# Kernel tuning notes

Measured on AMD Instinct MI355X. Metric: run time of the kernel, lower is better.

## Reference

```python
import jax, jax.numpy as jnp
import numpy as np
from jax import lax

B, H, W = 2, 384, 384
NF = 64
SECTIONS = [2, 3, 4, 5, 6, 7, 8]  # radial core widths -> kernel sizes 3,5,7,9,11,13,15


def _radial_matrix(w):
    """Static [K,K,w] matrix mapping w radial core channels -> full KxK kernel,
    K = 2*w-1, replicating the torch nested-loop radial interpolation + flipcat."""
    mid = w - 1
    M = np.zeros((w, w, w), dtype=np.float32)
    for i in range(w):
        for j in range(w):
            d = np.sqrt(float((i - mid) ** 2 + (j - mid) ** 2))
            if d > mid:
                continue
            low, high = np.floor(d), np.ceil(d)
            if low == high:
                M[i, j, int(low)] = 1.0
            else:
                M[i, j, int(low)] = high - d
                M[i, j, int(low) + 1] = d - low
    # flipcat along both spatial dims: index order [0..w-1, w-2..0]
    q = mid - np.abs(np.arange(2 * w - 1) - mid)
    return M[q][:, q]  # [K, K, w]


def _conv(x, w, b):
    y = lax.conv_general_dilated(x, w, (1, 1), 'SAME',
                                 dimension_numbers=('NCHW', 'OIHW', 'NCHW'))
    return y + b[None, :, None, None]


def _resblock(x, wa, ba, wb, bb):
    return x + _conv(jax.nn.relu(_conv(x, wa, ba)), wb, bb)


def setup_inputs() -> dict:
    key = jax.random.key(0)
    ks = jax.random.split(key, 12)

    def wgt(k, shape):
        fan_in = shape[1] * shape[2] * shape[3]
        return jax.random.normal(k, shape, jnp.float32) / np.sqrt(fan_in)

    inp = {
        'data_with_est': jax.random.normal(ks[0], (B, 2, H, W), jnp.float32),
        'data': jax.random.normal(ks[1], (B, 1, H, W), jnp.float32),
        'w_first': wgt(ks[2], (NF, 2, 3, 3)), 'b_first': jnp.zeros((NF,), jnp.float32),
        'w1a': wgt(ks[3], (NF, NF, 3, 3)), 'b1a': jnp.zeros((NF,), jnp.float32),
        'w1b': wgt(ks[4], (NF, NF, 3, 3)), 'b1b': jnp.zeros((NF,), jnp.float32),
        'w2a': wgt(ks[5], (NF, NF, 3, 3)), 'b2a': jnp.zeros((NF,), jnp.float32),
        'w2b': wgt(ks[6], (NF, NF, 3, 3)), 'b2b': jnp.zeros((NF,), jnp.float32),
        'w3a': wgt(ks[7], (NF, NF, 3, 3)), 'b3a': jnp.zeros((NF,), jnp.float32),
        'w3b': wgt(ks[8], (NF, NF, 3, 3)), 'b3b': jnp.zeros((NF,), jnp.float32),
        'w_out': wgt(ks[9], (35, NF, 3, 3)), 'b_out': jnp.zeros((35,), jnp.float32),
    }
    return inp


def reference(data_with_est, data, w_first, b_first, w1a, b1a, w1b, b1b,
              w2a, b2a, w2b, b2b, w3a, b3a, w3b, b3b, w_out, b_out):
    # KPN backbone
    x = _conv(data_with_est, w_first, b_first)
    x = _resblock(x, w1a, b1a, w1b, b1b)
    x = _resblock(x, w2a, b2a, w2b, b2b)
    x = _resblock(x, w3a, b3a, w3b, b3b)
    core = _conv(x, w_out, b_out)  # [B, 35, H, W]

    frames = data[:, 0]  # [B, H, W]  (N=1, color=1)
    pred_img = jnp.zeros((B, H, W), core.dtype)
    off = 0
    for wsec in SECTIONS:
        K = 2 * wsec - 1
        r = K // 2
        M = jnp.asarray(_radial_matrix(wsec))  # [K, K, wsec]
        c = jnp.abs(lax.slice_in_dim(core, off, off + wsec, axis=1))  # [B, wsec, H, W]
        off += wsec
        # position-varying KxK kernel per pixel, softmax over the K*K taps
        kern = jnp.einsum('ijc,bchw->bijhw', M, c).reshape(B, K * K, H, W)
        kern = jax.nn.softmax(kern, axis=1)
        pad = jnp.pad(frames, ((0, 0), (r, r), (r, r)))
        # shifted neighborhood stack in torch loop order (i over rows, j over cols)
        patches = jnp.stack([pad[:, i:i + H, j:j + W]
                             for i in range(K) for j in range(K)], axis=1)
        pred_img = pred_img + jnp.sum(kern * patches, axis=1)
    return pred_img[:, None]  # [B, 1, H, W]
```

## Files before the change

kernel.cpp:

```cpp
#include <hip/hip_runtime.h>

#define HH 384
#define WW 384
#define BB 2

typedef unsigned short ushort_t;
typedef short  s16x8 __attribute__((ext_vector_type(8)));
typedef float  f32x4 __attribute__((ext_vector_type(4)));
typedef int    i32x4 __attribute__((ext_vector_type(4)));
typedef int    i32x2 __attribute__((ext_vector_type(2)));

union V16 { i32x4 i4; s16x8 v; ushort_t h[8]; };
union V8  { i32x2 i2; ushort_t h[4]; };

__device__ __forceinline__ ushort_t f2b(float f) {
    unsigned u = __builtin_bit_cast(unsigned, f);
    u += 0x7fffu + ((u >> 16) & 1u);
    return (ushort_t)(u >> 16);
}
__device__ __forceinline__ float b2f(ushort_t h) {
    return __builtin_bit_cast(float, ((unsigned)h) << 16);
}

struct WSrc { const float* p[8]; };

__global__ __launch_bounds__(256)
void repack_k(WSrc ws, ushort_t* __restrict__ Wd)
{
    const int idx = blockIdx.x * 256 + threadIdx.x;
    float val = 0.f;
    if (idx < 221184) {
        const int j = idx / 36864, rem = idx - j * 36864;
        const int i = rem & 7, lane = (rem >> 3) & 63;
        const int f = rem >> 9;
        const int mt = f & 3, st = f >> 2;
        const int t = st % 9, s = st / 9;
        const int co = mt * 16 + (lane & 15);
        const int ci = s * 32 + (lane >> 4) * 8 + i;
        val = ws.p[j][((size_t)(co * 64 + ci)) * 9 + t];
    } else if (idx < 248832) {
        const int rem = idx - 221184;
        const int i = rem & 7, lane = (rem >> 3) & 63;
        const int f = rem >> 9;
        const int mt = f % 3, st = f / 3;
        const int t = st % 9, s = st / 9;
        const int co = mt * 16 + (lane & 15);
        const int ci = s * 32 + (lane >> 4) * 8 + i;
        val = (co < 35) ? ws.p[6][((size_t)(co * 64 + ci)) * 9 + t] : 0.f;
    } else {
        const int rem = idx - 248832;
        const int i = rem & 7, lane = (rem >> 3) & 63;
        const int mt = rem >> 9;
        const int co = mt * 16 + (lane & 15);
        const int k = (lane >> 4) * 8 + i;
        if (k < 18) {
            const int ch = (k >= 9) ? 1 : 0;
            const int t = k - ch * 9;
            val = ws.p[7][((size_t)(co * 2 + ch)) * 9 + t];
        }
    }
    if (idx < 250880) Wd[idx] = f2b(val);
}

template<bool RELU, bool RES>
__global__ __launch_bounds__(256, 2)
void conv_mfma(const ushort_t* __restrict__ in, const ushort_t* __restrict__ wp,
               const float* __restrict__ bias, const ushort_t* __restrict__ res,
               ushort_t* __restrict__ out)
{
    __shared__ __align__(16) char smem[41472 + 36864];
    i32x4* s4 = (i32x4*)smem;
    i32x4* sw = (i32x4*)(smem + 41472);

    const int tid = threadIdx.x;
    const int x0 = blockIdx.x * 16, y0 = blockIdx.y * 16, b = blockIdx.z;
    const int lane = tid & 63, w4 = (tid >> 6) * 4;
    const int n = lane & 15, g = lane >> 4;

    {
        i32x4 ta[11];
#pragma unroll
        for (int k = 0; k < 11; ++k) {
            const int idx = tid + k * 256;
            ta[k] = 0;
            if (idx < 2592) {
                const int oct = idx & 7, p = idx >> 3;
                const int r = p / 18, xx = p - r * 18;
                const int gy = y0 - 1 + r, gx = x0 - 1 + xx;
                if ((unsigned)gy < HH && (unsigned)gx < WW)
                    ta[k] = *(const i32x4*)(in +
                        ((size_t)((b * HH + gy) * WW + gx)) * 64 + oct * 8);
            }
        }
        i32x4 tw[9];
#pragma unroll
        for (int k = 0; k < 9; ++k)
            tw[k] = *(const i32x4*)(wp + (size_t)(tid + k * 256) * 8);
#pragma unroll
        for (int k = 0; k < 11; ++k) {
            const int idx = tid + k * 256;
            if (idx < 2592) {
                const int oct = idx & 7, p = idx >> 3;
                const int r = p / 18, xx = p - r * 18;
                s4[(r * 8 + oct) * 18 + xx] = ta[k];
            }
        }
#pragma unroll
        for (int k = 0; k < 9; ++k)
            sw[tid + k * 256] = tw[k];
    }
    __syncthreads();

    f32x4 acc[4][4];
#pragma unroll
    for (int i = 0; i < 4; ++i)
#pragma unroll
        for (int j = 0; j < 4; ++j) acc[i][j] = 0.f;

    i32x4 pw[9];
#pragma unroll
    for (int k = 0; k < 9; ++k)
        pw[k] = *(const i32x4*)(wp + (size_t)(2304 + tid + k * 256) * 8);

#pragma unroll
    for (int t = 0; t < 9; ++t) {
        const int ky = t / 3, kx = t - ky * 3;
        V16 bf[4];
#pragma unroll
        for (int nt = 0; nt < 4; ++nt)
            bf[nt].i4 = s4[((w4 + nt + ky) * 8 + g) * 18 + (n + kx)];
#pragma unroll
        for (int mt = 0; mt < 4; ++mt) {
            V16 af; af.i4 = sw[(t * 4 + mt) * 64 + lane];
#pragma unroll
            for (int nt = 0; nt < 4; ++nt)
                acc[nt][mt] = __builtin_amdgcn_mfma_f32_16x16x32_bf16(
                    af.v, bf[nt].v, acc[nt][mt], 0, 0, 0);
        }
    }

    __syncthreads();
#pragma unroll
    for (int k = 0; k < 9; ++k)
        sw[tid + k * 256] = pw[k];
    __syncthreads();

#pragma unroll
    for (int t = 0; t < 9; ++t) {
        const int ky = t / 3, kx = t - ky * 3;
        V16 bf[4];
#pragma unroll
        for (int nt = 0; nt < 4; ++nt)
            bf[nt].i4 = s4[((w4 + nt + ky) * 8 + 4 + g) * 18 + (n + kx)];
#pragma unroll
        for (int mt = 0; mt < 4; ++mt) {
            V16 af; af.i4 = sw[(t * 4 + mt) * 64 + lane];
#pragma unroll
            for (int nt = 0; nt < 4; ++nt)
                acc[nt][mt] = __builtin_amdgcn_mfma_f32_16x16x32_bf16(
                    af.v, bf[nt].v, acc[nt][mt], 0, 0, 0);
        }
    }

    __syncthreads();
#pragma unroll
    for (int nt = 0; nt < 4; ++nt) {
        const int row = w4 + nt;
#pragma unroll
        for (int mt = 0; mt < 4; ++mt) {
            const int co0 = mt * 16 + g * 4;
            const float4 bv = *(const float4*)(bias + co0);
            float vv[4] = {acc[nt][mt][0] + bv.x, acc[nt][mt][1] + bv.y,
                           acc[nt][mt][2] + bv.z, acc[nt][mt][3] + bv.w};
            V8 ov;
#pragma unroll
            for (int r = 0; r < 4; ++r)
                ov.h[r] = f2b(RELU ? fmaxf(vv[r], 0.f) : vv[r]);
            const int c = 2 * mt + (g >> 1);
            const int cpr = c ^ (n & 7);
            *(i32x2*)(smem + row * 2048 + n * 128 + cpr * 16 + (g & 1) * 8) = ov.i2;
        }
    }
    __syncthreads();
#pragma unroll
    for (int r0 = 0; r0 < 4; ++r0) {
        const int row = w4 + r0, y = y0 + row;
#pragma unroll
        for (int j = 0; j < 2; ++j) {
            const int px = (lane >> 3) + 8 * j;
            const int clin = lane & 7;
            const int cpr = clin ^ (px & 7);
            V16 v;
            v.i4 = *(const i32x4*)(smem + row * 2048 + px * 128 + cpr * 16);
            const size_t goff = ((size_t)((b * HH + y) * WW + x0 + px)) * 64
                                + clin * 8;
            if (RES) {
                V16 rv;
                rv.i4 = *(const i32x4*)(res + goff);
#pragma unroll
                for (int e = 0; e < 8; ++e)
                    v.h[e] = f2b(b2f(v.h[e]) + b2f(rv.h[e]));
            }
            *(i32x4*)(out + goff) = v.i4;
        }
    }
}

__global__ __launch_bounds__(256, 4)
void conv_first(const float* __restrict__ in, const ushort_t* __restrict__ wp,
                const float* __restrict__ bias, ushort_t* __restrict__ out)
{
    __shared__ float s_raw[2][18][20];
    __shared__ __align__(16) char epi[32768];
    const int tid = threadIdx.x;
    const int x0 = blockIdx.x * 16, y0 = blockIdx.y * 16, b = blockIdx.z;
    {
        float tmp[3];
#pragma unroll
        for (int k = 0; k < 3; ++k) {
            const int idx = tid + k * 256;
            tmp[k] = 0.f;
            if (idx < 648) {
                const int ch = idx / 324, rem = idx - ch * 324;
                const int r = rem / 18, x = rem - r * 18;
                const int gy = y0 - 1 + r, gx = x0 - 1 + x;
                if ((unsigned)gy < HH && (unsigned)gx < WW)
                    tmp[k] = in[((size_t)((b * 2 + ch) * HH + gy)) * WW + gx];
            }
        }
#pragma unroll
        for (int k = 0; k < 3; ++k) {
            const int idx = tid + k * 256;
            if (idx < 648) {
                const int ch = idx / 324, rem = idx - ch * 324;
                const int r = rem / 18, x = rem - r * 18;
                s_raw[ch][r][x] = tmp[k];
            }
        }
    }
    __syncthreads();

    const int lane = tid & 63, w4 = (tid >> 6) * 4;
    const int n = lane & 15, g = lane >> 4;

    V16 af[4];
#pragma unroll
    for (int mt = 0; mt < 4; ++mt)
        af[mt].i4 = *(const i32x4*)(wp + ((size_t)(mt * 64 + lane)) * 8);

    f32x4 acc[4][4];
#pragma unroll
    for (int i = 0; i < 4; ++i)
#pragma unroll
        for (int j = 0; j < 4; ++j) acc[i][j] = 0.f;

#pragma unroll
    for (int nt = 0; nt < 4; ++nt) {
        const int r = w4 + nt;
        V16 bf;
#pragma unroll
        for (int i = 0; i < 8; ++i) {
            const int k = g * 8 + i;
            float v = 0.f;
            if (k < 18) {
                const int ch = (k >= 9) ? 1 : 0;
                const int t = k - ch * 9;
                const int ky = t / 3, kx = t - ky * 3;
                v = s_raw[ch][r + ky][n + kx];
            }
            bf.h[i] = f2b(v);
        }
#pragma unroll
        for (int mt = 0; mt < 4; ++mt)
            acc[nt][mt] = __builtin_amdgcn_mfma_f32_16x16x32_bf16(
                af[mt].v, bf.v, acc[nt][mt], 0, 0, 0);
    }

#pragma unroll
    for (int nt = 0; nt < 4; ++nt) {
        const int row = w4 + nt;
#pragma unroll
        for (int mt = 0; mt < 4; ++mt) {
            const int co0 = mt * 16 + g * 4;
            const float4 bv = *(const float4*)(bias + co0);
            V8 ov;
            ov.h[0] = f2b(acc[nt][mt][0] + bv.x);
            ov.h[1] = f2b(acc[nt][mt][1] + bv.y);
            ov.h[2] = f2b(acc[nt][mt][2] + bv.z);
            ov.h[3] = f2b(acc[nt][mt][3] + bv.w);
            const int c = 2 * mt + (g >> 1);
            const int cpr = c ^ (n & 7);
            *(i32x2*)(epi + row * 2048 + n * 128 + cpr * 16 + (g & 1) * 8) = ov.i2;
        }
    }
    __syncthreads();
#pragma unroll
    for (int r0 = 0; r0 < 4; ++r0) {
        const int row = w4 + r0, y = y0 + row;
#pragma unroll
        for (int j = 0; j < 2; ++j) {
            const int px = (lane >> 3) + 8 * j;
            const int clin = lane & 7;
            const int cpr = clin ^ (px & 7);
            i32x4 v = *(const i32x4*)(epi + row * 2048 + px * 128 + cpr * 16);
            *(i32x4*)(out + ((size_t)((b * HH + y) * WW + x0 + px)) * 64
                          + clin * 8) = v;
        }
    }
}

constexpr int isq_(int v) { int r = 0; while ((r + 1) * (r + 1) <= v) ++r; return r; }
constexpr double csqrt_(int x) {
    double g = x ? (double)x : 0.0;
    if (x) for (int i = 0; i < 80; ++i) g = 0.5 * (g + (double)x / g);
    return g;
}
constexpr int tapm_(int W, int d2) {
    const int R = W - 1; int c = 0;
    for (int di = -R; di <= R; ++di)
        for (int dj = -R; dj <= R; ++dj)
            if (di * di + dj * dj == d2) ++c;
    return c;
}
constexpr int nout_(int W) {
    const int R = W - 1; int c = 0;
    for (int di = -R; di <= R; ++di)
        for (int dj = -R; dj <= R; ++dj)
            if (di * di + dj * dj > R * R) ++c;
    return c;
}

template<int W, int D2, int DI>
struct DiSum {
    static constexpr int R = W - 1;
    static __device__ __forceinline__ float run(const float* s_f, int base) {
        float s = 0.f;
        constexpr int rem = D2 - DI * DI;
        if constexpr (rem >= 0) {
            constexpr int sj = isq_(rem >= 0 ? rem : 0);
            if constexpr (sj * sj == rem) {
                s += s_f[base + DI * 48 + sj];
                if constexpr (sj > 0) s += s_f[base + DI * 48 - sj];
            }
        }
        if constexpr (DI < R) s += DiSum<W, D2, DI + 1>::run(s_f, base);
        return s;
    }
};

template<int W, int OFF, int D2>
struct D2Loop {
    static __device__ __forceinline__ void run(const float* cv, const float* s_f,
                                               int base, float& num, float& den) {
        constexpr int m = tapm_(W, D2);
        if constexpr (m > 0) {
            constexpr int lo = isq_(D2);
            float v;
            if constexpr (lo * lo == D2) {
                v = cv[OFF + lo];
            } else {
                constexpr float fr = (float)(csqrt_(D2) - (double)lo);
                v = __builtin_fmaf(fr, cv[OFF + lo + 1] - cv[OFF + lo], cv[OFF + lo]);
            }
            const float e = __expf(v);
            const float S = DiSum<W, D2, -(W - 1)>::run(s_f, base);
            num = __builtin_fmaf(e, S, num);
            den = __builtin_fmaf((float)m, e, den);
        }
        if constexpr (D2 > 0)
            D2Loop<W, OFF, D2 - 1>::run(cv, s_f, base, num, den);
    }
};

template<int W, int OFF>
__device__ __forceinline__ float kpn_section(const float* cv, const float* s_f,
                                             int base)
{
    constexpr int R = W - 1, R2 = R * R;
    float sout = 0.f;
#pragma unroll
    for (int di = -R; di <= R; ++di)
#pragma unroll
        for (int dj = -R; dj <= R; ++dj)
            if (di * di + dj * dj > R2)
                sout += s_f[base + di * 48 + dj];
    float num = sout, den = (float)nout_(W);
    D2Loop<W, OFF, R2>::run(cv, s_f, base, num, den);
    return num / den;
}

__global__ __launch_bounds__(256, 2)
void conv_kpn(const ushort_t* __restrict__ in, const ushort_t* __restrict__ wp,
              const float* __restrict__ bias, const float* __restrict__ frames,
              float* __restrict__ out)
{
    __shared__ __align__(16) char smem[41472 + 5760 + 27648];
    i32x4* s4 = (i32x4*)smem;
    float* s_core = (float*)smem;
    float* s_f = (float*)(smem + 41472);
    i32x4* sw = (i32x4*)(smem + 41472 + 5760);

    const int tid = threadIdx.x;
    const int x0 = blockIdx.x * 16, y0 = blockIdx.y * 16, b = blockIdx.z;

    {
        i32x4 ta[11];
#pragma unroll
        for (int k = 0; k < 11; ++k) {
            const int idx = tid + k * 256;
            ta[k] = 0;
            if (idx < 2592) {
                const int oct = idx & 7, p = idx >> 3;
                const int r = p / 18, xx = p - r * 18;
                const int gy = y0 - 1 + r, gx = x0 - 1 + xx;
                if ((unsigned)gy < HH && (unsigned)gx < WW)
                    ta[k] = *(const i32x4*)(in +
                        ((size_t)((b * HH + gy) * WW + gx)) * 64 + oct * 8);
            }
        }
        float ff[4];
#pragma unroll
        for (int k = 0; k < 4; ++k) {
            const int idx = tid + k * 256;
            ff[k] = 0.f;
            if (idx < 900) {
                const int r = idx / 30, c = idx - r * 30;
                const int y = y0 - 7 + r, x = x0 - 7 + c;
                if ((unsigned)y < HH && (unsigned)x < WW)
                    ff[k] = frames[((size_t)b * HH + y) * WW + x];
            }
        }
        i32x4 tw[7];
#pragma unroll
        for (int k = 0; k < 7; ++k) {
            const int idx = tid + k * 256;
            tw[k] = 0;
            if (idx < 1728)
                tw[k] = *(const i32x4*)(wp + (size_t)idx * 8);
        }
#pragma unroll
        for (int k = 0; k < 11; ++k) {
            const int idx = tid + k * 256;
            if (idx < 2592) {
                const int oct = idx & 7, p = idx >> 3;
                const int r = p / 18, xx = p - r * 18;
                s4[(r * 8 + oct) * 18 + xx] = ta[k];
            }
        }
#pragma unroll
        for (int k = 0; k < 4; ++k) {
            const int idx = tid + k * 256;
            if (idx < 900) {
                const int r = idx / 30, c = idx - r * 30;
                s_f[r * 48 + c] = ff[k];
            }
        }
#pragma unroll
        for (int k = 0; k < 7; ++k) {
            const int idx = tid + k * 256;
            if (idx < 1728) sw[idx] = tw[k];
        }
    }
    __syncthreads();

    const int lane = tid & 63, w4 = (tid >> 6) * 4;
    const int n = lane & 15, g = lane >> 4;

    f32x4 acc[4][3];
#pragma unroll
    for (int i = 0; i < 4; ++i)
#pragma unroll
        for (int j = 0; j < 3; ++j) acc[i][j] = 0.f;

    i32x4 pw[7];
#pragma unroll
    for (int k = 0; k < 7; ++k) {
        const int idx = tid + k * 256;
        pw[k] = 0;
        if (idx < 1728)
            pw[k] = *(const i32x4*)(wp + (size_t)(1728 + idx) * 8);
    }

#pragma unroll
    for (int t = 0; t < 9; ++t) {
        const int ky = t / 3, kx = t - ky * 3;
        V16 bf[4];
#pragma unroll
        for (int nt = 0; nt < 4; ++nt)
            bf[nt].i4 = s4[((w4 + nt + ky) * 8 + g) * 18 + (n + kx)];
#pragma unroll
        for (int mt = 0; mt < 3; ++mt) {
            V16 af; af.i4 = sw[(t * 3 + mt) * 64 + lane];
#pragma unroll
            for (int nt = 0; nt < 4; ++nt)
                acc[nt][mt] = __builtin_amdgcn_mfma_f32_16x16x32_bf16(
                    af.v, bf[nt].v, acc[nt][mt], 0, 0, 0);
        }
    }

    __syncthreads();
#pragma unroll
    for (int k = 0; k < 7; ++k) {
        const int idx = tid + k * 256;
        if (idx < 1728) sw[idx] = pw[k];
    }
    __syncthreads();

#pragma unroll
    for (int t = 0; t < 9; ++t) {
        const int ky = t / 3, kx = t - ky * 3;
        V16 bf[4];
#pragma unroll
        for (int nt = 0; nt < 4; ++nt)
            bf[nt].i4 = s4[((w4 + nt + ky) * 8 + 4 + g) * 18 + (n + kx)];
#pragma unroll
        for (int mt = 0; mt < 3; ++mt) {
            V16 af; af.i4 = sw[(t * 3 + mt) * 64 + lane];
#pragma unroll
            for (int nt = 0; nt < 4; ++nt)
                acc[nt][mt] = __builtin_amdgcn_mfma_f32_16x16x32_bf16(
                    af.v, bf[nt].v, acc[nt][mt], 0, 0, 0);
        }
    }

    __syncthreads();
#pragma unroll
    for (int nt = 0; nt < 4; ++nt) {
        const int px = (w4 + nt) * 16 + n;
#pragma unroll
        for (int mt = 0; mt < 3; ++mt) {
#pragma unroll
            for (int r = 0; r < 4; ++r) {
                const int ch = mt * 16 + g * 4 + r;
                if (ch < 35)
                    s_core[px * 37 + ch] = fabsf(acc[nt][mt][r] + bias[ch]);
            }
        }
    }
    __syncthreads();

    const int ty = tid >> 4, tx = tid & 15;
    const int base = (ty + 7) * 48 + (tx + 7);
    const float* cv = s_core + tid * 37;
    float pred = 0.f;
    pred += kpn_section<2, 0>(cv, s_f, base);
    pred += kpn_section<3, 2>(cv, s_f, base);
    pred += kpn_section<4, 5>(cv, s_f, base);
    pred += kpn_section<5, 9>(cv, s_f, base);
    pred += kpn_section<6, 14>(cv, s_f, base);
    pred += kpn_section<7, 20>(cv, s_f, base);
    pred += kpn_section<8, 27>(cv, s_f, base);
    out[((size_t)b * HH + y0 + ty) * WW + x0 + tx] = pred;
}

extern "C" void kernel_launch(void* const* d_in, const int* in_sizes, int n_in,
                              void* d_out, int out_size, void* d_ws, size_t ws_size,
                              hipStream_t stream)
{
    const float* est     = (const float*)d_in[0];
    const float* data    = (const float*)d_in[1];
    const float* w_first = (const float*)d_in[2];
    const float* b_first = (const float*)d_in[3];
    const float* w1a = (const float*)d_in[4];
    const float* b1a = (const float*)d_in[5];
    const float* w1b = (const float*)d_in[6];
    const float* b1b = (const float*)d_in[7];
    const float* w2a = (const float*)d_in[8];
    const float* b2a = (const float*)d_in[9];
    const float* w2b = (const float*)d_in[10];
    const float* b2b = (const float*)d_in[11];
    const float* w3a = (const float*)d_in[12];
    const float* b3a = (const float*)d_in[13];
    const float* w3b = (const float*)d_in[14];
    const float* b3b = (const float*)d_in[15];
    const float* w_out = (const float*)d_in[16];
    const float* b_out = (const float*)d_in[17];

    ushort_t* X  = (ushort_t*)d_ws;
    ushort_t* T  = X + (size_t)BB * HH * WW * 64;
    ushort_t* Wd = T + (size_t)BB * HH * WW * 64;

    WSrc wsrc;
    wsrc.p[0] = w1a; wsrc.p[1] = w1b; wsrc.p[2] = w2a; wsrc.p[3] = w2b;
    wsrc.p[4] = w3a; wsrc.p[5] = w3b; wsrc.p[6] = w_out; wsrc.p[7] = w_first;

    dim3 blk(256), g(WW / 16, HH / 16, BB);
    repack_k<<<980, 256, 0, stream>>>(wsrc, Wd);
    conv_first<<<g, blk, 0, stream>>>(est, Wd + 248832, b_first, X);
    conv_mfma<true,  false><<<g, blk, 0, stream>>>(X, Wd + 0,      b1a, nullptr, T);
    conv_mfma<false, true ><<<g, blk, 0, stream>>>(T, Wd + 36864,  b1b, X, X);
    conv_mfma<true,  false><<<g, blk, 0, stream>>>(X, Wd + 73728,  b2a, nullptr, T);
    conv_mfma<false, true ><<<g, blk, 0, stream>>>(T, Wd + 110592, b2b, X, X);
    conv_mfma<true,  false><<<g, blk, 0, stream>>>(X, Wd + 147456, b3a, nullptr, T);
    conv_mfma<false, true ><<<g, blk, 0, stream>>>(T, Wd + 184320, b3b, X, X);
    conv_kpn<<<g, blk, 0, stream>>>(X, Wd + 221184, b_out, data, (float*)d_out);
}
```

Before: 316.7 us.

## Stream conv weights through smaller LDS buffer in tap groups to raise occupancy

The weight staging buffer in LDS is shrunk from holding nine taps to holding one ky-row of three taps (or two taps in the KPN conv). Each group is refilled from a register prefetch between barriers. This cuts shared memory per block so the launch bounds can request three blocks per CU instead of two. The trade-off is many more block-wide barriers and more frequent global weight loads interleaved with the MFMA loop.

```diff
diff --git a/kernel.cpp b/kernel.cpp
--- a/kernel.cpp
+++ b/kernel.cpp
@@ -63,19 +63,19 @@
 }
 
 template<bool RELU, bool RES>
-__global__ __launch_bounds__(256, 2)
+__global__ __launch_bounds__(256, 3)
 void conv_mfma(const ushort_t* __restrict__ in, const ushort_t* __restrict__ wp,
                const float* __restrict__ bias, const ushort_t* __restrict__ res,
                ushort_t* __restrict__ out)
 {
-    __shared__ __align__(16) char smem[41472 + 36864];
+    __shared__ __align__(16) char smem[41472 + 12288];
     i32x4* s4 = (i32x4*)smem;
     i32x4* sw = (i32x4*)(smem + 41472);
 
     const int tid = threadIdx.x;
     const int x0 = blockIdx.x * 16, y0 = blockIdx.y * 16, b = blockIdx.z;
     const int lane = tid & 63, w4 = (tid >> 6) * 4;
-    const int n = lane & 15, g = lane >> 4;
+    const int n = lane & 15, q = lane >> 4;
 
     {
         i32x4 ta[11];
@@ -92,9 +92,9 @@
                         ((size_t)((b * HH + gy) * WW + gx)) * 64 + oct * 8);
             }
         }
-        i32x4 tw[9];
-#pragma unroll
-        for (int k = 0; k < 9; ++k)
+        i32x4 tw[3];
+#pragma unroll
+        for (int k = 0; k < 3; ++k)
             tw[k] = *(const i32x4*)(wp + (size_t)(tid + k * 256) * 8);
 #pragma unroll
         for (int k = 0; k < 11; ++k) {
@@ -106,7 +106,7 @@
             }
         }
 #pragma unroll
-        for (int k = 0; k < 9; ++k)
+        for (int k = 0; k < 3; ++k)
             sw[tid + k * 256] = tw[k];
     }
     __syncthreads();
@@ -117,48 +117,41 @@
 #pragma unroll
         for (int j = 0; j < 4; ++j) acc[i][j] = 0.f;
 
-    i32x4 pw[9];
-#pragma unroll
-    for (int k = 0; k < 9; ++k)
-        pw[k] = *(const i32x4*)(wp + (size_t)(2304 + tid + k * 256) * 8);
-
-#pragma unroll
-    for (int t = 0; t < 9; ++t) {
-        const int ky = t / 3, kx = t - ky * 3;
-        V16 bf[4];
-#pragma unroll
-        for (int nt = 0; nt < 4; ++nt)
-            bf[nt].i4 = s4[((w4 + nt + ky) * 8 + g) * 18 + (n + kx)];
-#pragma unroll
-        for (int mt = 0; mt < 4; ++mt) {
-            V16 af; af.i4 = sw[(t * 4 + mt) * 64 + lane];
+    i32x4 pw[3];
+#pragma unroll
+    for (int k = 0; k < 3; ++k)
+        pw[k] = *(const i32x4*)(wp + (size_t)(768 + tid + k * 256) * 8);
+
+#pragma unroll
+    for (int grp = 0; grp < 6; ++grp) {
+        const int s = grp / 3, ky = grp - s * 3;
+#pragma unroll
+        for (int kx = 0; kx < 3; ++kx) {
+            V16 bf[4];
 #pragma unroll
             for (int nt = 0; nt < 4; ++nt)
-                acc[nt][mt] = __builtin_amdgcn_mfma_f32_16x16x32_bf16(
-                    af.v, bf[nt].v, acc[nt][mt], 0, 0, 0);
-        }
-    }
-
-    __syncthreads();
-#pragma unroll
-    for (int k = 0; k < 9; ++k)
-        sw[tid + k * 256] = pw[k];
-    __syncthreads();
-
-#pragma unroll
-    for (int t = 0; t < 9; ++t) {
-        const int ky = t / 3, kx = t - ky * 3;
-        V16 bf[4];
-#pragma unroll
-        for (int nt = 0; nt < 4; ++nt)
-            bf[nt].i4 = s4[((w4 + nt + ky) * 8 + 4 + g) * 18 + (n + kx)];
-#pragma unroll
-        for (int mt = 0; mt < 4; ++mt) {
-            V16 af; af.i4 = sw[(t * 4 + mt) * 64 + lane];
-#pragma unroll
-            for (int nt = 0; nt < 4; ++nt)
-                acc[nt][mt] = __builtin_amdgcn_mfma_f32_16x16x32_bf16(
-                    af.v, bf[nt].v, acc[nt][mt], 0, 0, 0);
+                bf[nt].i4 = s4[((w4 + nt + ky) * 8 + s * 4 + q) * 18 + (n + kx)];
+#pragma unroll
+            for (int mt = 0; mt < 4; ++mt) {
+                V16 af; af.i4 = sw[(kx * 4 + mt) * 64 + lane];
+#pragma unroll
+                for (int nt = 0; nt < 4; ++nt)
+                    acc[nt][mt] = __builtin_amdgcn_mfma_f32_16x16x32_bf16(
+                        af.v, bf[nt].v, acc[nt][mt], 0, 0, 0);
+            }
+        }
+        if (grp < 5) {
+            __syncthreads();
+#pragma unroll
+            for (int k = 0; k < 3; ++k)
+                sw[tid + k * 256] = pw[k];
+            if (grp < 4) {
+#pragma unroll
+                for (int k = 0; k < 3; ++k)
+                    pw[k] = *(const i32x4*)(wp +
+                        (size_t)(768 * (grp + 2) + tid + k * 256) * 8);
+            }
+            __syncthreads();
         }
     }
 
@@ -168,7 +161,7 @@
         const int row = w4 + nt;
 #pragma unroll
         for (int mt = 0; mt < 4; ++mt) {
-            const int co0 = mt * 16 + g * 4;
+            const int co0 = mt * 16 + q * 4;
             const float4 bv = *(const float4*)(bias + co0);
             float vv[4] = {acc[nt][mt][0] + bv.x, acc[nt][mt][1] + bv.y,
                            acc[nt][mt][2] + bv.z, acc[nt][mt][3] + bv.w};
@@ -176,9 +169,9 @@
 #pragma unroll
             for (int r = 0; r < 4; ++r)
                 ov.h[r] = f2b(RELU ? fmaxf(vv[r], 0.f) : vv[r]);
-            const int c = 2 * mt + (g >> 1);
+            const int c = 2 * mt + (q >> 1);
             const int cpr = c ^ (n & 7);
-            *(i32x2*)(smem + row * 2048 + n * 128 + cpr * 16 + (g & 1) * 8) = ov.i2;
+            *(i32x2*)(smem + row * 2048 + n * 128 + cpr * 16 + (q & 1) * 8) = ov.i2;
         }
     }
     __syncthreads();
@@ -241,7 +234,7 @@
     __syncthreads();
 
     const int lane = tid & 63, w4 = (tid >> 6) * 4;
-    const int n = lane & 15, g = lane >> 4;
+    const int n = lane & 15, q = lane >> 4;
 
     V16 af[4];
 #pragma unroll
@@ -260,7 +253,7 @@
         V16 bf;
 #pragma unroll
         for (int i = 0; i < 8; ++i) {
-            const int k = g * 8 + i;
+            const int k = q * 8 + i;
             float v = 0.f;
             if (k < 18) {
                 const int ch = (k >= 9) ? 1 : 0;
@@ -281,16 +274,16 @@
         const int row = w4 + nt;
 #pragma unroll
         for (int mt = 0; mt < 4; ++mt) {
-            const int co0 = mt * 16 + g * 4;
+            const int co0 = mt * 16 + q * 4;
             const float4 bv = *(const float4*)(bias + co0);
             V8 ov;
             ov.h[0] = f2b(acc[nt][mt][0] + bv.x);
             ov.h[1] = f2b(acc[nt][mt][1] + bv.y);
             ov.h[2] = f2b(acc[nt][mt][2] + bv.z);
             ov.h[3] = f2b(acc[nt][mt][3] + bv.w);
-            const int c = 2 * mt + (g >> 1);
+            const int c = 2 * mt + (q >> 1);
             const int cpr = c ^ (n & 7);
-            *(i32x2*)(epi + row * 2048 + n * 128 + cpr * 16 + (g & 1) * 8) = ov.i2;
+            *(i32x2*)(epi + row * 2048 + n * 128 + cpr * 16 + (q & 1) * 8) = ov.i2;
         }
     }
     __syncthreads();
@@ -389,12 +382,12 @@
     return num / den;
 }
 
-__global__ __launch_bounds__(256, 2)
+__global__ __launch_bounds__(256, 3)
 void conv_kpn(const ushort_t* __restrict__ in, const ushort_t* __restrict__ wp,
               const float* __restrict__ bias, const float* __restrict__ frames,
               float* __restrict__ out)
 {
-    __shared__ __align__(16) char smem[41472 + 5760 + 27648];
+    __shared__ __align__(16) char smem[41472 + 5760 + 6144];
     i32x4* s4 = (i32x4*)smem;
     float* s_core = (float*)smem;
     float* s_f = (float*)(smem + 41472);
@@ -430,12 +423,12 @@
                     ff[k] = frames[((size_t)b * HH + y) * WW + x];
             }
         }
-        i32x4 tw[7];
-#pragma unroll
-        for (int k = 0; k < 7; ++k) {
+        i32x4 tw[2];
+#pragma unroll
+        for (int k = 0; k < 2; ++k) {
             const int idx = tid + k * 256;
             tw[k] = 0;
-            if (idx < 1728)
+            if (idx < 384)
                 tw[k] = *(const i32x4*)(wp + (size_t)idx * 8);
         }
 #pragma unroll
@@ -456,15 +449,15 @@
             }
         }
 #pragma unroll
-        for (int k = 0; k < 7; ++k) {
-            const int idx = tid + k * 256;
-            if (idx < 1728) sw[idx] = tw[k];
+        for (int k = 0; k < 2; ++k) {
+            const int idx = tid + k * 256;
+            if (idx < 384) sw[idx] = tw[k];
         }
     }
     __syncthreads();
 
     const int lane = tid & 63, w4 = (tid >> 6) * 4;
-    const int n = lane & 15, g = lane >> 4;
+    const int n = lane & 15, q = lane >> 4;
 
     f32x4 acc[4][3];
 #pragma unroll
@@ -472,54 +465,53 @@
 #pragma unroll
         for (int j = 0; j < 3; ++j) acc[i][j] = 0.f;
 
-    i32x4 pw[7];
-#pragma unroll
-    for (int k = 0; k < 7; ++k) {
+    i32x4 pw[2];
+#pragma unroll
+    for (int k = 0; k < 2; ++k) {
         const int idx = tid + k * 256;
         pw[k] = 0;
-        if (idx < 1728)
-            pw[k] = *(const i32x4*)(wp + (size_t)(1728 + idx) * 8);
-    }
-
-#pragma unroll
-    for (int t = 0; t < 9; ++t) {
-        const int ky = t / 3, kx = t - ky * 3;
-        V16 bf[4];
-#pragma unroll
-        for (int nt = 0; nt < 4; ++nt)
-            bf[nt].i4 = s4[((w4 + nt + ky) * 8 + g) * 18 + (n + kx)];
-#pragma unroll
-        for (int mt = 0; mt < 3; ++mt) {
-            V16 af; af.i4 = sw[(t * 3 + mt) * 64 + lane];
+        if (idx < 384)
+            pw[k] = *(const i32x4*)(wp + (size_t)(384 + idx) * 8);
+    }
+
+#pragma unroll
+    for (int grp = 0; grp < 9; ++grp) {
+#pragma unroll
+        for (int uu = 0; uu < 2; ++uu) {
+            const int u = grp * 2 + uu;
+            const int s = u / 9, t = u - s * 9;
+            const int ky = t / 3, kx = t - ky * 3;
+            V16 bf[4];
 #pragma unroll
             for (int nt = 0; nt < 4; ++nt)
-                acc[nt][mt] = __builtin_amdgcn_mfma_f32_16x16x32_bf16(
-                    af.v, bf[nt].v, acc[nt][mt], 0, 0, 0);
-        }
-    }
-
-    __syncthreads();
-#pragma unroll
-    for (int k = 0; k < 7; ++k) {
-        const int idx = tid + k * 256;
-        if (idx < 1728) sw[idx] = pw[k];
-    }
-    __syncthreads();
-
-#pragma unroll
-    for (int t = 0; t < 9; ++t) {
-        const int ky = t / 3, kx = t - ky * 3;
-        V16 bf[4];
-#pragma unroll
-        for (int nt = 0; nt < 4; ++nt)
-            bf[nt].i4 = s4[((w4 + nt + ky) * 8 + 4 + g) * 18 + (n + kx)];
-#pragma unroll
-        for (int mt = 0; mt < 3; ++mt) {
-            V16 af; af.i4 = sw[(t * 3 + mt) * 64 + lane];
-#pragma unroll
-            for (int nt = 0; nt < 4; ++nt)
-                acc[nt][mt] = __builtin_amdgcn_mfma_f32_16x16x32_bf16(
-                    af.v, bf[nt].v, acc[nt][mt], 0, 0, 0);
+                bf[nt].i4 = s4[((w4 + nt + ky) * 8 + s * 4 + q) * 18 + (n + kx)];
+#pragma unroll
+            for (int mt = 0; mt < 3; ++mt) {
+                V16 af; af.i4 = sw[uu * 192 + mt * 64 + lane];
+#pragma unroll
+                for (int nt = 0; nt < 4; ++nt)
+                    acc[nt][mt] = __builtin_amdgcn_mfma_f32_16x16x32_bf16(
+                        af.v, bf[nt].v, acc[nt][mt], 0, 0, 0);
+            }
+        }
+        if (grp < 8) {
+            __syncthreads();
+#pragma unroll
+            for (int k = 0; k < 2; ++k) {
+                const int idx = tid + k * 256;
+                if (idx < 384) sw[idx] = pw[k];
+            }
+            if (grp < 7) {
+#pragma unroll
+                for (int k = 0; k < 2; ++k) {
+                    const int idx = tid + k * 256;
+                    pw[k] = 0;
+                    if (idx < 384)
+                        pw[k] = *(const i32x4*)(wp +
+                            (size_t)(384 * (grp + 2) + idx) * 8);
+                }
+            }
+            __syncthreads();
         }
     }
 
@@ -531,7 +523,7 @@
         for (int mt = 0; mt < 3; ++mt) {
 #pragma unroll
             for (int r = 0; r < 4; ++r) {
-                const int ch = mt * 16 + g * 4 + r;
+                const int ch = mt * 16 + q * 4 + r;
                 if (ch < 35)
                     s_core[px * 37 + ch] = fabsf(acc[nt][mt][r] + bias[ch]);
             }
```

Result: slower. 392.7 us (+24.0%).

## Share symmetric ring neighbor sums across all KPN sections

Applied to the files above, without the earlier changes.

Restructures the per-pixel KPN filtering so that sums of frame values over each symmetric (m,k) ring are computed once and reused by all seven kernel-size sections, rather than recomputed per section and per distance. Each section accumulates exp-weighted numerator and denominator terms from the shared ring sums. This cuts redundant shared-memory loads and adds of the frame neighborhood in exchange for more live registers (14 accumulators plus exponentials). The rest of the change only renames the lane-group variable.

```diff
diff --git a/kernel.cpp b/kernel.cpp
--- a/kernel.cpp
+++ b/kernel.cpp
@@ -75,7 +75,7 @@
     const int tid = threadIdx.x;
     const int x0 = blockIdx.x * 16, y0 = blockIdx.y * 16, b = blockIdx.z;
     const int lane = tid & 63, w4 = (tid >> 6) * 4;
-    const int n = lane & 15, g = lane >> 4;
+    const int n = lane & 15, q = lane >> 4;
 
     {
         i32x4 ta[11];
@@ -128,7 +128,7 @@
         V16 bf[4];
 #pragma unroll
         for (int nt = 0; nt < 4; ++nt)
-            bf[nt].i4 = s4[((w4 + nt + ky) * 8 + g) * 18 + (n + kx)];
+            bf[nt].i4 = s4[((w4 + nt + ky) * 8 + q) * 18 + (n + kx)];
 #pragma unroll
         for (int mt = 0; mt < 4; ++mt) {
             V16 af; af.i4 = sw[(t * 4 + mt) * 64 + lane];
@@ -151,7 +151,7 @@
         V16 bf[4];
 #pragma unroll
         for (int nt = 0; nt < 4; ++nt)
-            bf[nt].i4 = s4[((w4 + nt + ky) * 8 + 4 + g) * 18 + (n + kx)];
+            bf[nt].i4 = s4[((w4 + nt + ky) * 8 + 4 + q) * 18 + (n + kx)];
 #pragma unroll
         for (int mt = 0; mt < 4; ++mt) {
             V16 af; af.i4 = sw[(t * 4 + mt) * 64 + lane];
@@ -168,7 +168,7 @@
         const int row = w4 + nt;
 #pragma unroll
         for (int mt = 0; mt < 4; ++mt) {
-            const int co0 = mt * 16 + g * 4;
+            const int co0 = mt * 16 + q * 4;
             const float4 bv = *(const float4*)(bias + co0);
             float vv[4] = {acc[nt][mt][0] + bv.x, acc[nt][mt][1] + bv.y,
                            acc[nt][mt][2] + bv.z, acc[nt][mt][3] + bv.w};
@@ -176,9 +176,9 @@
 #pragma unroll
             for (int r = 0; r < 4; ++r)
                 ov.h[r] = f2b(RELU ? fmaxf(vv[r], 0.f) : vv[r]);
-            const int c = 2 * mt + (g >> 1);
+            const int c = 2 * mt + (q >> 1);
             const int cpr = c ^ (n & 7);
-            *(i32x2*)(smem + row * 2048 + n * 128 + cpr * 16 + (g & 1) * 8) = ov.i2;
+            *(i32x2*)(smem + row * 2048 + n * 128 + cpr * 16 + (q & 1) * 8) = ov.i2;
         }
     }
     __syncthreads();
@@ -241,7 +241,7 @@
     __syncthreads();
 
     const int lane = tid & 63, w4 = (tid >> 6) * 4;
-    const int n = lane & 15, g = lane >> 4;
+    const int n = lane & 15, q = lane >> 4;
 
     V16 af[4];
 #pragma unroll
@@ -260,7 +260,7 @@
         V16 bf;
 #pragma unroll
         for (int i = 0; i < 8; ++i) {
-            const int k = g * 8 + i;
+            const int k = q * 8 + i;
             float v = 0.f;
             if (k < 18) {
                 const int ch = (k >= 9) ? 1 : 0;
@@ -281,16 +281,16 @@
         const int row = w4 + nt;
 #pragma unroll
         for (int mt = 0; mt < 4; ++mt) {
-            const int co0 = mt * 16 + g * 4;
+            const int co0 = mt * 16 + q * 4;
             const float4 bv = *(const float4*)(bias + co0);
             V8 ov;
             ov.h[0] = f2b(acc[nt][mt][0] + bv.x);
             ov.h[1] = f2b(acc[nt][mt][1] + bv.y);
             ov.h[2] = f2b(acc[nt][mt][2] + bv.z);
             ov.h[3] = f2b(acc[nt][mt][3] + bv.w);
-            const int c = 2 * mt + (g >> 1);
+            const int c = 2 * mt + (q >> 1);
             const int cpr = c ^ (n & 7);
-            *(i32x2*)(epi + row * 2048 + n * 128 + cpr * 16 + (g & 1) * 8) = ov.i2;
+            *(i32x2*)(epi + row * 2048 + n * 128 + cpr * 16 + (q & 1) * 8) = ov.i2;
         }
     }
     __syncthreads();
@@ -315,79 +315,84 @@
     if (x) for (int i = 0; i < 80; ++i) g = 0.5 * (g + (double)x / g);
     return g;
 }
-constexpr int tapm_(int W, int d2) {
-    const int R = W - 1; int c = 0;
-    for (int di = -R; di <= R; ++di)
-        for (int dj = -R; dj <= R; ++dj)
-            if (di * di + dj * dj == d2) ++c;
-    return c;
-}
-constexpr int nout_(int W) {
-    const int R = W - 1; int c = 0;
-    for (int di = -R; di <= R; ++di)
-        for (int dj = -R; dj <= R; ++dj)
-            if (di * di + dj * dj > R * R) ++c;
-    return c;
-}
-
-template<int W, int D2, int DI>
-struct DiSum {
-    static constexpr int R = W - 1;
-    static __device__ __forceinline__ float run(const float* s_f, int base) {
-        float s = 0.f;
-        constexpr int rem = D2 - DI * DI;
-        if constexpr (rem >= 0) {
-            constexpr int sj = isq_(rem >= 0 ? rem : 0);
-            if constexpr (sj * sj == rem) {
-                s += s_f[base + DI * 48 + sj];
-                if constexpr (sj > 0) s += s_f[base + DI * 48 - sj];
-            }
-        }
-        if constexpr (DI < R) s += DiSum<W, D2, DI + 1>::run(s_f, base);
-        return s;
+constexpr int ringmult_(int m, int k) {
+    if (m == 0) return 1;
+    if (k == 0 || k == m) return 4;
+    return 8;
+}
+constexpr int OFFS_(int s) {
+    return s == 0 ? 0 : s == 1 ? 2 : s == 2 ? 5 : s == 3 ? 9
+         : s == 4 ? 14 : s == 5 ? 20 : 27;
+}
+
+template<int M, int K>
+__device__ __forceinline__ float ringsum(const float* s_f, int base)
+{
+    if constexpr (M == 0) {
+        return s_f[base];
+    } else if constexpr (K == 0) {
+        return s_f[base + M * 48] + s_f[base - M * 48]
+             + s_f[base + M]      + s_f[base - M];
+    } else if constexpr (K == M) {
+        return s_f[base + M * 48 + M] + s_f[base + M * 48 - M]
+             + s_f[base - M * 48 + M] + s_f[base - M * 48 - M];
+    } else {
+        return s_f[base + M * 48 + K] + s_f[base + M * 48 - K]
+             + s_f[base - M * 48 + K] + s_f[base - M * 48 - K]
+             + s_f[base + K * 48 + M] + s_f[base + K * 48 - M]
+             + s_f[base - K * 48 + M] + s_f[base - K * 48 - M];
+    }
+}
+
+template<int M, int K, int S>
+struct SecAcc {
+    static __device__ __forceinline__ void run(const float* cv, float Sv,
+                                               float* num, float* den) {
+        constexpr int R = S + 1;
+        if constexpr (R >= M) {
+            constexpr int d2 = M * M + K * K;
+            constexpr int mult = ringmult_(M, K);
+            constexpr int OFF = OFFS_(S);
+            if constexpr (d2 <= R * R) {
+                constexpr int lo = isq_(d2);
+                float v;
+                if constexpr (lo * lo == d2) {
+                    v = cv[OFF + lo];
+                } else {
+                    constexpr float fr = (float)(csqrt_(d2) - (double)lo);
+                    v = __builtin_fmaf(fr, cv[OFF + lo + 1] - cv[OFF + lo],
+                                       cv[OFF + lo]);
+                }
+                const float e = __expf(v);
+                num[S] = __builtin_fmaf(e, Sv, num[S]);
+                den[S] = __builtin_fmaf((float)mult, e, den[S]);
+            } else {
+                num[S] += Sv;
+                den[S] += (float)mult;
+            }
+        }
+        if constexpr (S < 6) SecAcc<M, K, S + 1>::run(cv, Sv, num, den);
     }
 };
 
-template<int W, int OFF, int D2>
-struct D2Loop {
+template<int M, int K>
+struct RingK {
     static __device__ __forceinline__ void run(const float* cv, const float* s_f,
-                                               int base, float& num, float& den) {
-        constexpr int m = tapm_(W, D2);
-        if constexpr (m > 0) {
-            constexpr int lo = isq_(D2);
-            float v;
-            if constexpr (lo * lo == D2) {
-                v = cv[OFF + lo];
-            } else {
-                constexpr float fr = (float)(csqrt_(D2) - (double)lo);
-                v = __builtin_fmaf(fr, cv[OFF + lo + 1] - cv[OFF + lo], cv[OFF + lo]);
-            }
-            const float e = __expf(v);
-            const float S = DiSum<W, D2, -(W - 1)>::run(s_f, base);
-            num = __builtin_fmaf(e, S, num);
-            den = __builtin_fmaf((float)m, e, den);
-        }
-        if constexpr (D2 > 0)
-            D2Loop<W, OFF, D2 - 1>::run(cv, s_f, base, num, den);
+                                               int base, float* num, float* den) {
+        const float Sv = ringsum<M, K>(s_f, base);
+        SecAcc<M, K, 0>::run(cv, Sv, num, den);
+        if constexpr (K < M) RingK<M, K + 1>::run(cv, s_f, base, num, den);
     }
 };
 
-template<int W, int OFF>
-__device__ __forceinline__ float kpn_section(const float* cv, const float* s_f,
-                                             int base)
-{
-    constexpr int R = W - 1, R2 = R * R;
-    float sout = 0.f;
-#pragma unroll
-    for (int di = -R; di <= R; ++di)
-#pragma unroll
-        for (int dj = -R; dj <= R; ++dj)
-            if (di * di + dj * dj > R2)
-                sout += s_f[base + di * 48 + dj];
-    float num = sout, den = (float)nout_(W);
-    D2Loop<W, OFF, R2>::run(cv, s_f, base, num, den);
-    return num / den;
-}
+template<int M>
+struct RingLoop {
+    static __device__ __forceinline__ void run(const float* cv, const float* s_f,
+                                               int base, float* num, float* den) {
+        RingK<M, 0>::run(cv, s_f, base, num, den);
+        if constexpr (M < 7) RingLoop<M + 1>::run(cv, s_f, base, num, den);
+    }
+};
 
 __global__ __launch_bounds__(256, 2)
 void conv_kpn(const ushort_t* __restrict__ in, const ushort_t* __restrict__ wp,
@@ -464,7 +469,7 @@
     __syncthreads();
 
     const int lane = tid & 63, w4 = (tid >> 6) * 4;
-    const int n = lane & 15, g = lane >> 4;
+    const int n = lane & 15, q = lane >> 4;
 
     f32x4 acc[4][3];
 #pragma unroll
@@ -487,7 +492,7 @@
         V16 bf[4];
 #pragma unroll
         for (int nt = 0; nt < 4; ++nt)
-            bf[nt].i4 = s4[((w4 + nt + ky) * 8 + g) * 18 + (n + kx)];
+            bf[nt].i4 = s4[((w4 + nt + ky) * 8 + q) * 18 + (n + kx)];
 #pragma unroll
         for (int mt = 0; mt < 3; ++mt) {
             V16 af; af.i4 = sw[(t * 3 + mt) * 64 + lane];
@@ -512,7 +517,7 @@
         V16 bf[4];
 #pragma unroll
         for (int nt = 0; nt < 4; ++nt)
-            bf[nt].i4 = s4[((w4 + nt + ky) * 8 + 4 + g) * 18 + (n + kx)];
+            bf[nt].i4 = s4[((w4 + nt + ky) * 8 + 4 + q) * 18 + (n + kx)];
 #pragma unroll
         for (int mt = 0; mt < 3; ++mt) {
             V16 af; af.i4 = sw[(t * 3 + mt) * 64 + lane];
@@ -531,7 +536,7 @@
         for (int mt = 0; mt < 3; ++mt) {
 #pragma unroll
             for (int r = 0; r < 4; ++r) {
-                const int ch = mt * 16 + g * 4 + r;
+                const int ch = mt * 16 + q * 4 + r;
                 if (ch < 35)
                     s_core[px * 37 + ch] = fabsf(acc[nt][mt][r] + bias[ch]);
             }
@@ -542,14 +547,15 @@
     const int ty = tid >> 4, tx = tid & 15;
     const int base = (ty + 7) * 48 + (tx + 7);
     const float* cv = s_core + tid * 37;
+
+    float num[7], den[7];
+#pragma unroll
+    for (int s = 0; s < 7; ++s) { num[s] = 0.f; den[s] = 0.f; }
+    RingLoop<0>::run(cv, s_f, base, num, den);
     float pred = 0.f;
-    pred += kpn_section<2, 0>(cv, s_f, base);
-    pred += kpn_section<3, 2>(cv, s_f, base);
-    pred += kpn_section<4, 5>(cv, s_f, base);
-    pred += kpn_section<5, 9>(cv, s_f, base);
-    pred += kpn_section<6, 14>(cv, s_f, base);
-    pred += kpn_section<7, 20>(cv, s_f, base);
-    pred += kpn_section<8, 27>(cv, s_f, base);
+#pragma unroll
+    for (int s = 0; s < 7; ++s) pred += num[s] / den[s];
+
     out[((size_t)b * HH + y0 + ty) * WW + x0 + tx] = pred;
 }
 
```

Result: no change. 316.4 us, median of 3 (-0.1%).
